# Kernel tuning notes

Measured on AMD Instinct MI355X. Metric: run time of the kernel, lower is better.

## Reference

```python
import jax, jax.numpy as jnp
import numpy as np

EPS_DENOM = 1e-7   # epsilon added to sigmoid-sum denominator in the torch code
EPS_NORM = 1e-5    # torch InstanceNorm1d default eps


def _fcnn(x, W1, b1, W2, b2):
    # FCNN: Linear -> ReLU -> Linear
    return jax.nn.relu(x @ W1 + b1) @ W2 + b2


def setup_inputs() -> dict:
    key = jax.random.key(0)
    N, E, D, H = 100000, 1600000, 32, 128  # nodes, edges, feature dim (c_in1=c_out2), hidden (c_out1)
    ks = jax.random.split(key, 11)
    node_features = jax.random.normal(ks[0], (N, D), jnp.float32)
    edge_features = jax.random.normal(ks[1], (E, D), jnp.float32)
    edge_index = jax.random.randint(ks[2], (2, E), 0, N, dtype=jnp.int64)
    sD = 1.0 / np.sqrt(D)
    sH = 1.0 / np.sqrt(H)
    # FCNN_one params
    W1a = jax.random.normal(ks[3], (D, H), jnp.float32) * sD
    b1a = jax.random.normal(ks[4], (H,), jnp.float32) * sD
    W2a = jax.random.normal(ks[5], (H, D), jnp.float32) * sH
    b2a = jax.random.normal(ks[6], (D,), jnp.float32) * sH
    # FCNN_two params
    W1b = jax.random.normal(ks[7], (D, H), jnp.float32) * sD
    b1b = jax.random.normal(ks[8], (H,), jnp.float32) * sD
    W2b = jax.random.normal(ks[9], (H, D), jnp.float32) * sH
    b2b = jax.random.normal(ks[10], (D,), jnp.float32) * sH
    return dict(node_features=node_features, edge_features=edge_features,
                W1a=W1a, b1a=b1a, W2a=W2a, b2a=b2a,
                W1b=W1b, b1b=b1b, W2b=W2b, b2b=b2b,
                edge_index=edge_index)


def reference(node_features, edge_features, W1a, b1a, W2a, b2a,
              W1b, b1b, W2b, b2b, edge_index):
    x = node_features                      # [N, D]
    N = x.shape[0]
    h1 = _fcnn(x, W1a, b1a, W2a, b2a)      # FCNN_one(x_i) for all nodes
    h2 = _fcnn(x, W1b, b1b, W2b, b2b)      # FCNN_two(x_j) for all nodes

    s = jax.nn.sigmoid(edge_features)      # [E, D]
    # node i gathers edges where it is src OR dst (both directions)
    seg = jnp.concatenate([edge_index[0], edge_index[1]])  # [2E] center node
    nbr = jnp.concatenate([edge_index[1], edge_index[0]])  # [2E] neighbor node
    s2 = jnp.concatenate([s, s], axis=0)                   # [2E, D]

    denom = EPS_DENOM + jax.ops.segment_sum(s2, seg, num_segments=N)  # [N, D]
    msg = (s2 / denom[seg]) * h2[nbr]                                 # [2E, D]
    agg = jax.ops.segment_sum(msg, seg, num_segments=N)               # [N, D]

    h = h1 + agg
    # InstanceNorm1d over the feature dim (no affine, biased variance); dropout is identity (eval)
    mu = jnp.mean(h, axis=-1, keepdims=True)
    var = jnp.var(h, axis=-1, keepdims=True)
    hn = (h - mu) * jax.lax.rsqrt(var + EPS_NORM)
    return x + jax.nn.relu(hn)
```

## Files before the change

### kernel.cpp

```cpp
#include <hip/hip_runtime.h>

#define EPS_DENOM 1e-7f
#define EPS_NORM  1e-5f

static constexpr int D  = 32;
static constexpr int H  = 128;
static constexpr int BK = 128;
static constexpr int CHUNK = 1024;
static constexpr int CAPMAX = 6144;

typedef _Float16 f16x8 __attribute__((ext_vector_type(8)));
typedef float    f32x4 __attribute__((ext_vector_type(4)));

__global__ __launch_bounds__(256) void fcnn_mfma_kernel(
    const float* __restrict__ x,
    const float* __restrict__ W1a, const float* __restrict__ b1a,
    const float* __restrict__ W2a, const float* __restrict__ b2a,
    const float* __restrict__ W1b, const float* __restrict__ b1b,
    const float* __restrict__ W2b, const float* __restrict__ b2b,
    float* __restrict__ h1, _Float16* __restrict__ h2h, int N)
{
    __shared__ _Float16 lds[30208];
    _Float16* xk = lds;

    const int tid = threadIdx.x;
    const int nb0 = blockIdx.x * 64;

    #pragma unroll
    for (int t = 0; t < 8; ++t) {
        int f = t * 256 + tid;
        int node = f >> 5, off = f & 31;
        int gn = nb0 + node;
        float v = (gn < N) ? x[(size_t)gn * 32 + off] : 0.0f;
        xk[node * 40 + off] = (_Float16)v;
    }
    for (int fc = 0; fc < 2; ++fc) {
        const float* W1 = fc ? W1b : W1a;
        const float* W2 = fc ? W2b : W2a;
        _Float16* w1t = lds + 2560 + fc * 5120;
        _Float16* w2t = lds + 12800 + fc * 4352;
        #pragma unroll
        for (int t = 0; t < 16; ++t) {
            int f = t * 256 + tid;
            w1t[(f & 127) * 40 + (f >> 7)] = (_Float16)W1[f];
        }
        #pragma unroll
        for (int t = 0; t < 16; ++t) {
            int f = t * 256 + tid;
            w2t[(f & 31) * 136 + (f >> 5)] = (_Float16)W2[f];
        }
    }
    __syncthreads();

    const int wid  = tid >> 6;
    const int lane = tid & 63;
    const int m    = lane & 15;
    const int g    = lane >> 4;
    _Float16* t1 = lds + 21504 + wid * 2176;

    f16x8 ax = *(const f16x8*)(xk + (wid * 16 + m) * 40 + g * 8);

    for (int fc = 0; fc < 2; ++fc) {
        const float* b1v = fc ? b1b : b1a;
        const float* b2v = fc ? b2b : b2a;
        const _Float16* w1t = lds + 2560 + fc * 5120;
        const _Float16* w2t = lds + 12800 + fc * 4352;

        for (int hb = 0; hb < 8; ++hb) {
            f16x8 bw = *(const f16x8*)(w1t + (hb * 16 + m) * 40 + g * 8);
            f32x4 c = {0.f, 0.f, 0.f, 0.f};
            c = __builtin_amdgcn_mfma_f32_16x16x32_f16(ax, bw, c, 0, 0, 0);
            float bias = b1v[hb * 16 + m];
            #pragma unroll
            for (int r = 0; r < 4; ++r) {
                float tv = fmaxf(c[r] + bias, 0.0f);
                t1[(g * 4 + r) * 136 + hb * 16 + m] = (_Float16)tv;
            }
        }

        for (int dt = 0; dt < 2; ++dt) {
            f32x4 c2 = {0.f, 0.f, 0.f, 0.f};
            #pragma unroll
            for (int kc = 0; kc < 4; ++kc) {
                f16x8 a2  = *(const f16x8*)(t1 + m * 136 + kc * 32 + g * 8);
                f16x8 b2w = *(const f16x8*)(w2t + (dt * 16 + m) * 136 + kc * 32 + g * 8);
                c2 = __builtin_amdgcn_mfma_f32_16x16x32_f16(a2, b2w, c2, 0, 0, 0);
            }
            float bias = b2v[dt * 16 + m];
            #pragma unroll
            for (int r = 0; r < 4; ++r) {
                int gn = nb0 + wid * 16 + g * 4 + r;
                if (gn < N) {
                    float val = c2[r] + bias;
                    if (fc == 0) h1[(size_t)gn * 32 + dt * 16 + m] = val;
                    else         h2h[(size_t)gn * 32 + dt * 16 + m] = (_Float16)val;
                }
            }
        }
        __syncthreads();
    }
}

__global__ __launch_bounds__(256) void bin1_kernel(
    const int* __restrict__ ei, const float* __restrict__ ef,
    int* __restrict__ gcursor, uint2* __restrict__ gadj,
    unsigned char* __restrict__ pay, int E, int CAP, int paymode)
{
    __shared__ uint2 recs[2 * CHUNK];
    __shared__ uint4 srows4[CHUNK * 2];
    __shared__ int cnt[1024];
    __shared__ int offs[1024];
    __shared__ int gbase[1024];
    __shared__ int partial[256];

    const int tid  = threadIdx.x;
    const int base = blockIdx.x * CHUNK;
    const int ne   = min(CHUNK, E - base);

    #pragma unroll
    for (int i = 0; i < 4; ++i) cnt[tid * 4 + i] = 0;
    __syncthreads();

    int av[CHUNK / 256], bv[CHUNK / 256];
    #pragma unroll
    for (int j = 0; j < CHUNK / 256; ++j) {
        int r = j * 256 + tid;
        if (r < ne) {
            int e = base + r;
            av[j] = ei[e]; bv[j] = ei[E + e];
            atomicAdd(&cnt[av[j] >> 7], 1);
            atomicAdd(&cnt[bv[j] >> 7], 1);
        } else av[j] = -1;
    }

    if (paymode) {
        const float4* efc = (const float4*)(ef + (size_t)base * 32);
        uchar4* sc4 = (uchar4*)srows4;
        const int nf4 = ne * 8;
        #pragma unroll
        for (int j = 0; j < CHUNK * 8 / 256; ++j) {
            int fidx = j * 256 + tid;
            if (fidx < nf4) {
                float4 v = efc[fidx];
                uchar4 q;
                q.x = (unsigned char)(255.0f / (1.0f + __expf(-v.x)) + 0.5f);
                q.y = (unsigned char)(255.0f / (1.0f + __expf(-v.y)) + 0.5f);
                q.z = (unsigned char)(255.0f / (1.0f + __expf(-v.z)) + 0.5f);
                q.w = (unsigned char)(255.0f / (1.0f + __expf(-v.w)) + 0.5f);
                sc4[fidx] = q;
            }
        }
    }
    __syncthreads();

    int c0 = cnt[tid*4], c1 = cnt[tid*4+1], c2 = cnt[tid*4+2], c3 = cnt[tid*4+3];
    int psum = c0 + c1 + c2 + c3;
    partial[tid] = psum;
    __syncthreads();
    for (int off = 1; off < 256; off <<= 1) {
        int t = (tid >= off) ? partial[tid - off] : 0;
        __syncthreads();
        partial[tid] += t;
        __syncthreads();
    }
    int ex = partial[tid] - psum;
    offs[tid*4]   = ex;
    offs[tid*4+1] = ex + c0;
    offs[tid*4+2] = ex + c0 + c1;
    offs[tid*4+3] = ex + c0 + c1 + c2;
    cnt[tid*4]    = ex;
    cnt[tid*4+1]  = ex + c0;
    cnt[tid*4+2]  = ex + c0 + c1;
    cnt[tid*4+3]  = ex + c0 + c1 + c2;
    __syncthreads();

    #pragma unroll
    for (int j = 0; j < CHUNK / 256; ++j) {
        if (av[j] >= 0) {
            int e = base + j * 256 + tid;
            int a = av[j], b = bv[j];
            int pa = atomicAdd(&cnt[a >> 7], 1);
            recs[pa] = make_uint2(((unsigned)(a & 127) << 21) | (unsigned)e,
                                  ((unsigned)(a >> 7) << 17) | (unsigned)b);
            int pb = atomicAdd(&cnt[b >> 7], 1);
            recs[pb] = make_uint2(((unsigned)(b & 127) << 21) | (unsigned)e,
                                  ((unsigned)(b >> 7) << 17) | (unsigned)a);
        }
    }
    __syncthreads();

    #pragma unroll
    for (int i = 0; i < 4; ++i) {
        int bidx = tid * 4 + i;
        int c = cnt[bidx] - offs[bidx];
        if (c > 0) gbase[bidx] = atomicAdd(&gcursor[bidx], c);
    }
    __syncthreads();

    const unsigned char* srows = (const unsigned char*)srows4;
    int total = 2 * ne;
    for (int i = tid; i < total; i += 256) {
        uint2 r = recs[i];
        int bidx = r.y >> 17;
        int dest = gbase[bidx] + (i - offs[bidx]);
        if (dest < CAP) {
            size_t slot = (size_t)bidx * CAP + dest;
            gadj[slot] = r;
            if (paymode) {
                int le = (int)(r.x & 0x1FFFFFu) - base;
                const uint4* sr = (const uint4*)(srows + le * 32);
                uint4 s0 = sr[0], s1 = sr[1];
                uint4* pd = (uint4*)(pay + slot * 32);
                pd[0] = s0; pd[1] = s1;
            }
        }
    }
}

__global__ __launch_bounds__(256) void bin2_kernel(
    const int* __restrict__ gcursor, uint2* __restrict__ gadj,
    int* __restrict__ gstart, int* __restrict__ gdeg,
    int N, int CAP, int paymode)
{
    __shared__ uint2 recs[CAPMAX];
    __shared__ int cnt[BK];
    __shared__ int sc[BK];
    __shared__ int lcur[BK];

    const int tid = threadIdx.x;
    const int bk  = blockIdx.x;
    const int count = min(gcursor[bk], CAP);
    uint2* seg = gadj + (size_t)bk * CAP;

    if (tid < BK) cnt[tid] = 0;
    for (int i = tid; i < count; i += 256) recs[i] = seg[i];
    __syncthreads();

    for (int i = tid; i < count; i += 256)
        atomicAdd(&cnt[(recs[i].x >> 21) & 127], 1);
    __syncthreads();

    int v = (tid < BK) ? cnt[tid] : 0;
    if (tid < BK) sc[tid] = v;
    __syncthreads();
    for (int off = 1; off < BK; off <<= 1) {
        int t = (tid < BK && tid >= off) ? sc[tid - off] : 0;
        __syncthreads();
        if (tid < BK) sc[tid] += t;
        __syncthreads();
    }
    if (tid < BK) {
        int excl = sc[tid] - v;
        lcur[tid] = excl;
        int gn = bk * BK + tid;
        if (gn < N) {
            gstart[gn] = bk * CAP + excl;
            gdeg[gn]   = v;
        }
    }
    __syncthreads();

    for (int i = tid; i < count; i += 256) {
        uint2 r = recs[i];
        int l = (r.x >> 21) & 127;
        int pos = atomicAdd(&lcur[l], 1);
        unsigned xv = paymode ? (unsigned)i : (r.x & 0x1FFFFFu);
        seg[pos] = make_uint2(xv, r.y & 0x1FFFFu);
    }
}

template <int MODE>
__global__ __launch_bounds__(256) void gather_kernel(
    const float* __restrict__ x,  const float* __restrict__ ef,
    const unsigned char* __restrict__ pay,
    const float* __restrict__ h1, const _Float16* __restrict__ h2h,
    const int* __restrict__ gstart, const int* __restrict__ gdeg,
    const uint2* __restrict__ adj2,
    float* __restrict__ out, int N, int CAP)
{
    int t = blockIdx.x * blockDim.x + threadIdx.x;
    int n = t >> 5;
    int d = t & 31;
    if (n >= N) return;

    int start = gstart[n];
    int end   = start + gdeg[n];
    const unsigned char* payb = pay + (size_t)(n >> 7) * CAP * 32 + d;

    float s_sum = 0.0f, sh_sum = 0.0f;
    int k = start;
    for (; k + 4 <= end; k += 4) {
        uint2 r0 = adj2[k+0], r1 = adj2[k+1], r2 = adj2[k+2], r3 = adj2[k+3];
        float s0, s1, s2, s3;
        if (MODE) {
            s0 = (float)payb[(size_t)r0.x * 32] * (1.0f / 255.0f);
            s1 = (float)payb[(size_t)r1.x * 32] * (1.0f / 255.0f);
            s2 = (float)payb[(size_t)r2.x * 32] * (1.0f / 255.0f);
            s3 = (float)payb[(size_t)r3.x * 32] * (1.0f / 255.0f);
        } else {
            s0 = 1.0f / (1.0f + __expf(-ef[(size_t)r0.x * 32 + d]));
            s1 = 1.0f / (1.0f + __expf(-ef[(size_t)r1.x * 32 + d]));
            s2 = 1.0f / (1.0f + __expf(-ef[(size_t)r2.x * 32 + d]));
            s3 = 1.0f / (1.0f + __expf(-ef[(size_t)r3.x * 32 + d]));
        }
        float h0 = (float)h2h[(size_t)r0.y * 32 + d];
        float h1v = (float)h2h[(size_t)r1.y * 32 + d];
        float h2v = (float)h2h[(size_t)r2.y * 32 + d];
        float h3 = (float)h2h[(size_t)r3.y * 32 + d];
        s_sum += (s0 + s1) + (s2 + s3);
        sh_sum = fmaf(s0, h0, sh_sum);
        sh_sum = fmaf(s1, h1v, sh_sum);
        sh_sum = fmaf(s2, h2v, sh_sum);
        sh_sum = fmaf(s3, h3, sh_sum);
    }
    for (; k < end; ++k) {
        uint2 r = adj2[k];
        float s;
        if (MODE) s = (float)payb[(size_t)r.x * 32] * (1.0f / 255.0f);
        else      s = 1.0f / (1.0f + __expf(-ef[(size_t)r.x * 32 + d]));
        float hh = (float)h2h[(size_t)r.y * 32 + d];
        s_sum += s;
        sh_sum = fmaf(s, hh, sh_sum);
    }

    size_t idx = (size_t)n * 32 + d;
    float h = h1[idx] + sh_sum / (EPS_DENOM + s_sum);

    float sum = h, sq = h * h;
    #pragma unroll
    for (int off = 16; off > 0; off >>= 1) {
        sum += __shfl_xor(sum, off, 32);
        sq  += __shfl_xor(sq,  off, 32);
    }
    float mu  = sum * (1.0f / 32.0f);
    float var = fmaxf(sq * (1.0f / 32.0f) - mu * mu, 0.0f);
    float hn  = (h - mu) * rsqrtf(var + EPS_NORM);

    out[idx] = x[idx] + fmaxf(hn, 0.0f);
}

extern "C" void kernel_launch(void* const* d_in, const int* in_sizes, int n_in,
                              void* d_out, int out_size, void* d_ws, size_t ws_size,
                              hipStream_t stream)
{
    const float* x   = (const float*)d_in[0];
    const float* ef  = (const float*)d_in[1];
    const float* W1a = (const float*)d_in[2];
    const float* b1a = (const float*)d_in[3];
    const float* W2a = (const float*)d_in[4];
    const float* b2a = (const float*)d_in[5];
    const float* W1b = (const float*)d_in[6];
    const float* b1b = (const float*)d_in[7];
    const float* W2b = (const float*)d_in[8];
    const float* b2b = (const float*)d_in[9];
    const int*   ei  = (const int*)d_in[10];
    float* out = (float*)d_out;

    const int N  = in_sizes[0] / D;
    const int E  = in_sizes[1] / D;
    const int NB = (N + BK - 1) / BK;
    int CAP = (2 * E) / NB;
    CAP = CAP + CAP / 2;
    CAP = (CAP + 255) & ~255;
    if (CAP > CAPMAX) CAP = CAPMAX;

    char* p = (char*)d_ws;
    float*    h1      = (float*)p;    p += (size_t)N * 32 * 4;
    _Float16* h2h     = (_Float16*)p; p += (size_t)N * 32 * 2;
    int*      gcursor = (int*)p;      p += 1024 * 4;
    int*      gstart  = (int*)p;      p += (size_t)N * 4;
    int*      gdeg    = (int*)p;      p += (size_t)N * 4;
    p = (char*)(((uintptr_t)p + 31) & ~(uintptr_t)31);
    uint2*    gadj    = (uint2*)p;    p += (size_t)NB * CAP * 8;
    p = (char*)(((uintptr_t)p + 31) & ~(uintptr_t)31);
    unsigned char* pay = (unsigned char*)p;
    const bool use_pay =
        ((size_t)(p - (char*)d_ws) + (size_t)NB * CAP * 32) <= ws_size;
    const int paymode = use_pay ? 1 : 0;

    hipMemsetAsync(gcursor, 0, 1024 * 4, stream);

    fcnn_mfma_kernel<<<(N + 63) / 64, 256, 0, stream>>>(
        x, W1a, b1a, W2a, b2a, W1b, b1b, W2b, b2b, h1, h2h, N);

    bin1_kernel<<<(E + CHUNK - 1) / CHUNK, 256, 0, stream>>>(
        ei, ef, gcursor, gadj, pay, E, CAP, paymode);
    bin2_kernel<<<NB, 256, 0, stream>>>(gcursor, gadj, gstart, gdeg, N, CAP, paymode);

    int gthreads = N * 32;
    if (use_pay)
        gather_kernel<1><<<(gthreads + 255) / 256, 256, 0, stream>>>(
            x, ef, pay, h1, h2h, gstart, gdeg, gadj, out, N, CAP);
    else
        gather_kernel<0><<<(gthreads + 255) / 256, 256, 0, stream>>>(
            x, ef, pay, h1, h2h, gstart, gdeg, gadj, out, N, CAP);
}
```

Baseline: 652.3 us.

## Drop LDS staging of quantized edge sigmoids and triple bin1 chunk size

```diff
diff --git a/kernel.cpp b/kernel.cpp
--- a/kernel.cpp
+++ b/kernel.cpp
@@ -6,7 +6,7 @@
 static constexpr int D  = 32;
 static constexpr int H  = 128;
 static constexpr int BK = 128;
-static constexpr int CHUNK = 1024;
+static constexpr int CHUNK = 3072;
 static constexpr int CAPMAX = 6144;
 
 typedef _Float16 f16x8 __attribute__((ext_vector_type(8)));
@@ -107,7 +107,6 @@
     unsigned char* __restrict__ pay, int E, int CAP, int paymode)
 {
     __shared__ uint2 recs[2 * CHUNK];
-    __shared__ uint4 srows4[CHUNK * 2];
     __shared__ int cnt[1024];
     __shared__ int offs[1024];
     __shared__ int gbase[1024];
@@ -131,25 +130,6 @@
             atomicAdd(&cnt[av[j] >> 7], 1);
             atomicAdd(&cnt[bv[j] >> 7], 1);
         } else av[j] = -1;
-    }
-
-    if (paymode) {
-        const float4* efc = (const float4*)(ef + (size_t)base * 32);
-        uchar4* sc4 = (uchar4*)srows4;
-        const int nf4 = ne * 8;
-        #pragma unroll
-        for (int j = 0; j < CHUNK * 8 / 256; ++j) {
-            int fidx = j * 256 + tid;
-            if (fidx < nf4) {
-                float4 v = efc[fidx];
-                uchar4 q;
-                q.x = (unsigned char)(255.0f / (1.0f + __expf(-v.x)) + 0.5f);
-                q.y = (unsigned char)(255.0f / (1.0f + __expf(-v.y)) + 0.5f);
-                q.z = (unsigned char)(255.0f / (1.0f + __expf(-v.z)) + 0.5f);
-                q.w = (unsigned char)(255.0f / (1.0f + __expf(-v.w)) + 0.5f);
-                sc4[fidx] = q;
-            }
-        }
     }
     __syncthreads();
 
@@ -174,6 +154,7 @@
     cnt[tid*4+3]  = ex + c0 + c1 + c2;
     __syncthreads();
 
+    int pa_s[CHUNK / 256], pb_s[CHUNK / 256];
     #pragma unroll
     for (int j = 0; j < CHUNK / 256; ++j) {
         if (av[j] >= 0) {
@@ -185,6 +166,7 @@
             int pb = atomicAdd(&cnt[b >> 7], 1);
             recs[pb] = make_uint2(((unsigned)(b & 127) << 21) | (unsigned)e,
                                   ((unsigned)(b >> 7) << 17) | (unsigned)a);
+            pa_s[j] = pa; pb_s[j] = pb;
         }
     }
     __syncthreads();
@@ -197,21 +179,40 @@
     }
     __syncthreads();
 
-    const unsigned char* srows = (const unsigned char*)srows4;
     int total = 2 * ne;
     for (int i = tid; i < total; i += 256) {
         uint2 r = recs[i];
         int bidx = r.y >> 17;
         int dest = gbase[bidx] + (i - offs[bidx]);
-        if (dest < CAP) {
-            size_t slot = (size_t)bidx * CAP + dest;
-            gadj[slot] = r;
-            if (paymode) {
-                int le = (int)(r.x & 0x1FFFFFu) - base;
-                const uint4* sr = (const uint4*)(srows + le * 32);
-                uint4 s0 = sr[0], s1 = sr[1];
-                uint4* pd = (uint4*)(pay + slot * 32);
-                pd[0] = s0; pd[1] = s1;
+        if (dest < CAP)
+            gadj[(size_t)bidx * CAP + dest] = r;
+    }
+
+    if (paymode) {
+        #pragma unroll
+        for (int j = 0; j < CHUNK / 256; ++j) {
+            if (av[j] < 0) continue;
+            int e = base + j * 256 + tid;
+            const float4* er = (const float4*)(ef + (size_t)e * 32);
+            union { uchar4 q[8]; uint4 u[2]; } pk;
+            #pragma unroll
+            for (int u = 0; u < 8; ++u) {
+                float4 v = er[u];
+                pk.q[u].x = (unsigned char)(255.0f / (1.0f + __expf(-v.x)) + 0.5f);
+                pk.q[u].y = (unsigned char)(255.0f / (1.0f + __expf(-v.y)) + 0.5f);
+                pk.q[u].z = (unsigned char)(255.0f / (1.0f + __expf(-v.z)) + 0.5f);
+                pk.q[u].w = (unsigned char)(255.0f / (1.0f + __expf(-v.w)) + 0.5f);
+            }
+            int a = av[j], b = bv[j];
+            int da = gbase[a >> 7] + (pa_s[j] - offs[a >> 7]);
+            int db = gbase[b >> 7] + (pb_s[j] - offs[b >> 7]);
+            if (da < CAP) {
+                uint4* pd = (uint4*)(pay + ((size_t)(a >> 7) * CAP + da) * 32);
+                pd[0] = pk.u[0]; pd[1] = pk.u[1];
+            }
+            if (db < CAP) {
+                uint4* pd = (uint4*)(pay + ((size_t)(b >> 7) * CAP + db) * 32);
+                pd[0] = pk.u[0]; pd[1] = pk.u[1];
             }
         }
     }
```

Result: no change. 659.3 us (+1.1%).
